# Kernel optimization log

Measured on AMD Instinct MI355X. Metric: run time of the kernel, lower is better.

The kernel has to match this reference:

```python
import jax, jax.numpy as jnp
import numpy as np

N_TILES, NX = 6, 96
IN_C, HID_C = 128, 256
BATCH = 4


def _build_neighbors(n_tiles=N_TILES, nx=NX):
    # 4-connectivity on each tile with periodic wrap (fixed cubed-sphere-style
    # grid graph; preserves the gather/mean access pattern of build_dgl_graph).
    i, j = np.meshgrid(np.arange(nx), np.arange(nx), indexing='ij')
    idx = lambda ii, jj: (ii % nx) * nx + (jj % nx)
    per_tile = np.stack([idx(i - 1, j), idx(i + 1, j), idx(i, j - 1), idx(i, j + 1)],
                        axis=-1).reshape(nx * nx, 4)
    offsets = (np.arange(n_tiles) * nx * nx)[:, None, None]
    return (per_tile[None] + offsets).reshape(-1, 4).astype(np.int32)


def setup_inputs() -> dict:
    key = jax.random.key(0)
    ks = jax.random.split(key, 6)
    s = lambda fan_in: 1.0 / np.sqrt(fan_in)
    return {
        'x': jax.random.normal(ks[0], (BATCH, N_TILES, NX, NX, IN_C), jnp.float32),
        'neighbors': jnp.asarray(_build_neighbors()),
        'W_self1': jax.random.normal(ks[1], (IN_C, HID_C), jnp.float32) * s(IN_C),
        'W_neigh1': jax.random.normal(ks[2], (IN_C, HID_C), jnp.float32) * s(IN_C),
        'b1': jnp.zeros((HID_C,), jnp.float32),
        'W_self2': jax.random.normal(ks[3], (HID_C, HID_C), jnp.float32) * s(HID_C),
        'W_neigh2': jax.random.normal(ks[4], (HID_C, HID_C), jnp.float32) * s(HID_C),
        'b2': jnp.zeros((HID_C,), jnp.float32),
    }


def _sage_conv(h, neighbors, W_self, W_neigh, b):
    # h: [B, N, C]; neighbors: [N, 4] -> mean-aggregated SAGEConv
    h_neigh = jnp.mean(h[:, neighbors], axis=2)  # [B, N, 4, C] -> [B, N, C]
    return jnp.einsum('bnc,cd->bnd', h, W_self) + \
           jnp.einsum('bnc,cd->bnd', h_neigh, W_neigh) + b


def reference(x, neighbors, W_self1, W_neigh1, b1, W_self2, W_neigh2, b2):
    B, T, X, Y, C = x.shape
    h = x.reshape(B, T * X * Y, C)                      # flatten sphere -> nodes
    h = jax.nn.relu(_sage_conv(h, neighbors, W_self1, W_neigh1, b1))
    h = jax.nn.relu(_sage_conv(h, neighbors, W_self2, W_neigh2, b2))
    return h.reshape(B, T, X, Y, -1)
```

## Files before the change

### kernel.cpp

```cpp
#include <hip/hip_runtime.h>
#include <stdint.h>

typedef __attribute__((ext_vector_type(8))) short short8;
typedef __attribute__((ext_vector_type(4))) float f32x4;

#define NNODES 55296
#define DOUT 256

#define WAIT_VM(N) asm volatile("s_waitcnt vmcnt(" #N ")" ::: "memory")
#define SOFT_FENCE asm volatile("" ::: "memory")

__device__ __forceinline__ float bf2f(unsigned short h) {
    union { unsigned u; float f; } x; x.u = ((unsigned)h) << 16; return x.f;
}
__device__ __forceinline__ unsigned short f2bf(float f) {
    union { float f; unsigned u; } x; x.f = f;
    return (unsigned short)((x.u + 0x7fffu + ((x.u >> 16) & 1u)) >> 16);
}

__device__ __forceinline__ void storev(float* p, float v) { *p = v; }
__device__ __forceinline__ void storev(unsigned short* p, float v) { *p = f2bf(v); }

__device__ __forceinline__ void dma16(const void* g, void* l) {
    __builtin_amdgcn_global_load_lds(
        reinterpret_cast<const unsigned int __attribute__((address_space(1)))*>((uintptr_t)g),
        reinterpret_cast<unsigned int __attribute__((address_space(3)))*>((uintptr_t)l),
        16, 0, 0);
}

__device__ __forceinline__ short8 frag_self(const float* p) {
    float4 a = *(const float4*)p, b = *(const float4*)(p + 4);
    union { short8 s; unsigned short u[8]; } r;
    r.u[0] = f2bf(a.x); r.u[1] = f2bf(a.y); r.u[2] = f2bf(a.z); r.u[3] = f2bf(a.w);
    r.u[4] = f2bf(b.x); r.u[5] = f2bf(b.y); r.u[6] = f2bf(b.z); r.u[7] = f2bf(b.w);
    return r.s;
}
__device__ __forceinline__ short8 frag_self(const unsigned short* p) {
    return *(const short8*)p;
}
__device__ __forceinline__ void acc8(const float* p, float* o) {
    float4 a = *(const float4*)p, b = *(const float4*)(p + 4);
    o[0] += a.x; o[1] += a.y; o[2] += a.z; o[3] += a.w;
    o[4] += b.x; o[5] += b.y; o[6] += b.z; o[7] += b.w;
}
__device__ __forceinline__ void acc8(const unsigned short* p, float* o) {
    uint4 v = *(const uint4*)p;
    const unsigned short* u = (const unsigned short*)&v;
#pragma unroll
    for (int i = 0; i < 8; ++i) o[i] += bf2f(u[i]);
}
template <typename TIN>
__device__ __forceinline__ short8 frag_mean4(const TIN* p0, const TIN* p1,
                                             const TIN* p2, const TIN* p3) {
    float s[8] = {0.f, 0.f, 0.f, 0.f, 0.f, 0.f, 0.f, 0.f};
    acc8(p0, s); acc8(p1, s); acc8(p2, s); acc8(p3, s);
    union { short8 s8; unsigned short u[8]; } r;
#pragma unroll
    for (int i = 0; i < 8; ++i) r.u[i] = f2bf(s[i] * 0.25f);
    return r.s8;
}

__global__ void build_wt(const float* __restrict__ Ws,
                         const float* __restrict__ Wn,
                         unsigned short* __restrict__ Wt, int C) {
    int K2 = 2 * C;
    int idx = blockIdx.x * 256 + threadIdx.x;
    if (idx >= 256 * K2) return;
    int d = idx / K2;
    int k = idx - d * K2;
    float v = (k < C) ? Ws[(size_t)k * DOUT + d] : Wn[(size_t)(k - C) * DOUT + d];
    Wt[idx] = f2bf(v);
}

__global__ __launch_bounds__(256) void mean_xb(const float* __restrict__ x,
                                               const int* __restrict__ nbr,
                                               unsigned short* __restrict__ xm) {
    const int idx = blockIdx.x * 256 + threadIdx.x;
    const int node = idx >> 4;
    const int ch = (idx & 15) * 8;
    const int b = node / NNODES;
    const int n = node - b * NNODES;
    const size_t bbase = (size_t)b * NNODES;
    const int4 nb = *(const int4*)(nbr + (size_t)n * 4);
    const float* ps = x + (size_t)node * 128 + ch;
    union { uint4 v; unsigned short u[8]; } rs, rm;
    float4 a0 = *(const float4*)ps, a1 = *(const float4*)(ps + 4);
    rs.u[0] = f2bf(a0.x); rs.u[1] = f2bf(a0.y); rs.u[2] = f2bf(a0.z); rs.u[3] = f2bf(a0.w);
    rs.u[4] = f2bf(a1.x); rs.u[5] = f2bf(a1.y); rs.u[6] = f2bf(a1.z); rs.u[7] = f2bf(a1.w);
    float s[8] = {0.f, 0.f, 0.f, 0.f, 0.f, 0.f, 0.f, 0.f};
    acc8(x + (bbase + nb.x) * 128 + ch, s);
    acc8(x + (bbase + nb.y) * 128 + ch, s);
    acc8(x + (bbase + nb.z) * 128 + ch, s);
    acc8(x + (bbase + nb.w) * 128 + ch, s);
#pragma unroll
    for (int i = 0; i < 8; ++i) rm.u[i] = f2bf(s[i] * 0.25f);
    *(uint4*)(xm + (size_t)node * 256 + ch) = rs.v;
    *(uint4*)(xm + (size_t)node * 256 + 128 + ch) = rm.v;
}

template <int C, typename TIN>
__global__ __launch_bounds__(256) void mean_pass(const TIN* __restrict__ hin,
                                                 const int* __restrict__ nbr,
                                                 unsigned short* __restrict__ hm) {
    constexpr int CPL = C / 8;
    const int idx = blockIdx.x * 256 + threadIdx.x;
    const int node = idx / CPL;
    const int ch = (idx - node * CPL) * 8;
    const int b = node / NNODES;
    const int n = node - b * NNODES;
    const size_t bbase = (size_t)b * NNODES;
    const int4 nb = *(const int4*)(nbr + (size_t)n * 4);
    float s[8] = {0.f, 0.f, 0.f, 0.f, 0.f, 0.f, 0.f, 0.f};
    acc8(hin + (bbase + nb.x) * (size_t)C + ch, s);
    acc8(hin + (bbase + nb.y) * (size_t)C + ch, s);
    acc8(hin + (bbase + nb.z) * (size_t)C + ch, s);
    acc8(hin + (bbase + nb.w) * (size_t)C + ch, s);
    union { uint4 v; unsigned short u[8]; } r;
#pragma unroll
    for (int i = 0; i < 8; ++i) r.u[i] = f2bf(s[i] * 0.25f);
    *(uint4*)(hm + (size_t)node * C + ch) = r.v;
}

template <int NK, typename TOUT>
__global__ __launch_bounds__(256) void sage_v13(
    const unsigned short* __restrict__ h1p,
    const unsigned short* __restrict__ hmp,
    const unsigned short* __restrict__ Wt,
    const float* __restrict__ bias,
    TOUT* __restrict__ out,
    int nwg) {
    extern __shared__ char lds[];
    constexpr int WB = NK * 64;
    const int tid = threadIdx.x;
    const int bid = blockIdx.x;
    const int wk = (bid & 7) * (nwg >> 3) + (bid >> 3);
    const int yg = wk & 1;
    const int rb = wk >> 1;
    const int gcol0 = yg * 128;
    const int rowbase = rb * 128;

    const int l = tid & 63, w = tid >> 6;
    const int lr = l & 15, lg = l >> 4;
    const int rowg = w >> 1;
    const int colb = (w & 1) * 64;

    const char* wsrc = (const char*)Wt + (size_t)gcol0 * WB;

    auto stageW = [&](int q) {
        char* wb = lds + ((q & 1) << 14);
#pragma unroll
        for (int i = 0; i < 4; ++i) {
            int o = w * 1024 + i * 4096 + l * 16;
            int col = o >> 7, kq = o & 127;
            dma16(wsrc + (unsigned)(col * WB + q * 128 + (kq ^ ((col & 7) << 4))),
                  wb + o);
        }
    };
    auto issueA = [&](int p) {
        const char* base = (NK == 16 && p >= 8) ? (const char*)hmp : (const char*)h1p;
        const unsigned kb = (unsigned)(p & 7) * 64;
        char* ring = lds + 32768 + (p & 3) * 8192;
#pragma unroll
        for (int i = 0; i < 2; ++i) {
            const int cj = w + i * 4;
            const int row = rowbase + cj * 16 + lr;
            dma16(base + ((unsigned)row * 512 + kb + (unsigned)(lg << 4)),
                  ring + cj * 1024);
        }
    };

    stageW(0); issueA(0); issueA(1); issueA(2);

    f32x4 acc[4][4];
#pragma unroll
    for (int m = 0; m < 4; ++m)
#pragma unroll
        for (int j = 0; j < 4; ++j) acc[m][j] = (f32x4){0.f, 0.f, 0.f, 0.f};

    const int abase = rowg * 4096 + lg * 256 + lr * 16;

#pragma unroll
    for (int kk = 0; kk < NK; ++kk) {
        int n;
        if (kk == 0) n = 4;
        else if (kk & 1) n = ((kk + 1 < NK) ? 6 : 0) + ((kk + 2 < NK) ? 2 : 0);
        else n = 2 + ((kk + 2 < NK) ? 2 : 0);
        switch (n) {
            case 0: WAIT_VM(0); break;
            case 2: WAIT_VM(2); break;
            case 4: WAIT_VM(4); break;
            case 6: WAIT_VM(6); break;
            default: WAIT_VM(8); break;
        }
        __builtin_amdgcn_s_barrier();
        SOFT_FENCE;

        if (((kk & 1) == 0) && (kk + 2 < NK)) stageW((kk + 2) >> 1);
        if (kk + 3 < NK) issueA(kk + 3);

        const int bufo = 32768 + (kk & 3) * 8192;
        short8 af[4];
#pragma unroll
        for (int m = 0; m < 4; ++m)
            af[m] = *(const short8*)(lds + bufo + abase + m * 1024);

        char* wbuf = lds + (((kk >> 1) & 1) << 14);
        const int kq0 = ((kk & 1) << 6) | (lg << 4);
#pragma unroll
        for (int j = 0; j < 4; ++j) {
            const int col = colb + j * 16 + lr;
            const short8 wf = *(const short8*)(
                wbuf + (col << 7) + (kq0 ^ ((lr & 7) << 4)));
#pragma unroll
            for (int m = 0; m < 4; ++m)
                acc[m][j] = __builtin_amdgcn_mfma_f32_16x16x32_bf16(wf, af[m], acc[m][j], 0, 0, 0);
        }
        SOFT_FENCE;
    }

#pragma unroll
    for (int m = 0; m < 4; ++m) {
        const int row = rowbase + rowg * 64 + m * 16 + lr;
#pragma unroll
        for (int j = 0; j < 4; ++j) {
            const int gcol = gcol0 + colb + j * 16 + lg * 4;
            const float4 bv = *(const float4*)(bias + gcol);
            float o0 = fmaxf(acc[m][j][0] + bv.x, 0.f);
            float o1 = fmaxf(acc[m][j][1] + bv.y, 0.f);
            float o2 = fmaxf(acc[m][j][2] + bv.z, 0.f);
            float o3 = fmaxf(acc[m][j][3] + bv.w, 0.f);
            if constexpr (sizeof(TOUT) == 4) {
                float4 o = {o0, o1, o2, o3};
                *(float4*)((float*)out + (size_t)row * 256 + gcol) = o;
            } else {
                union { unsigned short u[4]; uint2 v; } pk;
                pk.u[0] = f2bf(o0); pk.u[1] = f2bf(o1);
                pk.u[2] = f2bf(o2); pk.u[3] = f2bf(o3);
                *(uint2*)((unsigned short*)out + (size_t)row * 256 + gcol) = pk.v;
            }
        }
    }
}

template <int C, typename TIN, typename TOUT>
__global__ __launch_bounds__(512, 2) void sage_v3(
    const TIN* __restrict__ hin, const int* __restrict__ nbr,
    const unsigned short* __restrict__ Wt, const float* __restrict__ bias,
    TOUT* __restrict__ out) {
    constexpr int K2 = 2 * C;
    constexpr int ROWB = K2 * 2;
    constexpr int LCOLS = 131072 / ROWB;
    constexpr int CG = LCOLS / 128;
    constexpr int RG = 8 / CG;
    extern __shared__ char Bs[];

    const int tid = threadIdx.x;
    const int gcol0 = blockIdx.y * LCOLS;
    {
        const char* src = (const char*)(Wt + (size_t)gcol0 * K2);
#pragma unroll
        for (int i = 0; i < 16; ++i) {
            int byt = (i * 512 + tid) * 16;
            uint4 v = *(const uint4*)(src + byt);
            int c = byt / ROWB;
            *(uint4*)(Bs + (byt ^ ((c & 7) << 4))) = v;
        }
    }
    __syncthreads();

    const int l = tid & 63;
    const int w = tid >> 6;
    const int rowg = w / CG;
    const int colb = (w % CG) * 128;
    const int lr = l & 15, lg = l >> 4;

    const int rowbase = blockIdx.x * (RG * 64) + rowg * 64;
    const int bb = rowbase / NNODES;
    const int n0 = rowbase - bb * NNODES;
    const size_t bbase = (size_t)bb * NNODES;

    unsigned soff[4], noff[4][4];
#pragma unroll
    for (int m = 0; m < 4; ++m) {
        int r = m * 16 + lr;
        soff[m] = (unsigned)(((rowbase + r) * (size_t)C + lg * 8) * sizeof(TIN));
        int4 nb = *(const int4*)(nbr + (size_t)(n0 + r) * 4);
        noff[m][0] = (unsigned)(((bbase + nb.x) * C + lg * 8) * sizeof(TIN));
        noff[m][1] = (unsigned)(((bbase + nb.y) * C + lg * 8) * sizeof(TIN));
        noff[m][2] = (unsigned)(((bbase + nb.z) * C + lg * 8) * sizeof(TIN));
        noff[m][3] = (unsigned)(((bbase + nb.w) * C + lg * 8) * sizeof(TIN));
    }
    const char* hb = (const char*)hin;

    f32x4 acc[4][8];
#pragma unroll
    for (int m = 0; m < 4; ++m)
#pragma unroll
        for (int j = 0; j < 8; ++j) acc[m][j] = (f32x4){0.f, 0.f, 0.f, 0.f};

#pragma unroll
    for (int kk = 0; kk < K2 / 32; ++kk) {
        const int k0 = kk * 32;
        short8 a[4];
        if (k0 < C) {
            const unsigned kb = k0 * sizeof(TIN);
#pragma unroll
            for (int m = 0; m < 4; ++m)
                a[m] = frag_self((const TIN*)(hb + soff[m] + kb));
        } else {
            const unsigned kb = (k0 - C) * sizeof(TIN);
#pragma unroll
            for (int m = 0; m < 4; ++m)
                a[m] = frag_mean4((const TIN*)(hb + noff[m][0] + kb),
                                  (const TIN*)(hb + noff[m][1] + kb),
                                  (const TIN*)(hb + noff[m][2] + kb),
                                  (const TIN*)(hb + noff[m][3] + kb));
        }
#pragma unroll
        for (int j = 0; j < 8; ++j) {
            const int c = colb + j * 16 + lr;
            const short8 bf = *(const short8*)(
                Bs + ((c * ROWB + (k0 + lg * 8) * 2) ^ ((l & 7) << 4)));
#pragma unroll
            for (int m = 0; m < 4; ++m)
                acc[m][j] = __builtin_amdgcn_mfma_f32_16x16x32_bf16(a[m], bf, acc[m][j], 0, 0, 0);
        }
    }

#pragma unroll
    for (int j = 0; j < 8; ++j) {
        const int gcol = gcol0 + colb + j * 16 + lr;
        const float bv = bias[gcol];
#pragma unroll
        for (int m = 0; m < 4; ++m) {
#pragma unroll
            for (int r = 0; r < 4; ++r) {
                const int row = rowbase + m * 16 + lg * 4 + r;
                storev(out + (size_t)row * DOUT + gcol, fmaxf(acc[m][j][r] + bv, 0.f));
            }
        }
    }
}

extern "C" void kernel_launch(void* const* d_in, const int* in_sizes, int n_in,
                              void* d_out, int out_size, void* d_ws, size_t ws_size,
                              hipStream_t stream) {
    const float* x = (const float*)d_in[0];
    const int* nbr = (const int*)d_in[1];
    const float* Ws1 = (const float*)d_in[2];
    const float* Wn1 = (const float*)d_in[3];
    const float* b1 = (const float*)d_in[4];
    const float* Ws2 = (const float*)d_in[5];
    const float* Wn2 = (const float*)d_in[6];
    const float* b2 = (const float*)d_in[7];
    float* out = (float*)d_out;

    const int B = in_sizes[0] / (NNODES * 128);
    const int M = B * NNODES;

    char* ws = (char*)d_ws;
    const size_t h1_bytes = (size_t)M * DOUT * 2;
    const size_t hm_bytes = (size_t)M * DOUT * 2;
    const size_t need = h1_bytes + hm_bytes + 131072 + 262144;

    if (ws_size >= need) {
        unsigned short* h1 = (unsigned short*)ws;
        unsigned short* xm = (unsigned short*)(ws + h1_bytes);
        unsigned short* Wt1 = (unsigned short*)(ws + h1_bytes + hm_bytes);
        unsigned short* Wt2 = Wt1 + 256 * 256;

        build_wt<<<256, 256, 0, stream>>>(Ws1, Wn1, Wt1, 128);
        build_wt<<<512, 256, 0, stream>>>(Ws2, Wn2, Wt2, 256);

        hipFuncSetAttribute((const void*)sage_v13<8, unsigned short>,
                            hipFuncAttributeMaxDynamicSharedMemorySize, 65536);
        hipFuncSetAttribute((const void*)sage_v13<16, float>,
                            hipFuncAttributeMaxDynamicSharedMemorySize, 65536);

        const int nwg = (M / 128) * 2;

        mean_xb<<<M / 16, 256, 0, stream>>>(x, nbr, xm);
        sage_v13<8, unsigned short>
            <<<nwg, 256, 65536, stream>>>(xm, xm, Wt1, b1, h1, nwg);
        mean_pass<256, unsigned short><<<M * 32 / 256, 256, 0, stream>>>(h1, nbr, xm);
        sage_v13<16, float>
            <<<nwg, 256, 65536, stream>>>(h1, xm, Wt2, b2, out, nwg);
    } else {
        unsigned short* h1 = (unsigned short*)ws;
        unsigned short* Wt1 = (unsigned short*)(ws + h1_bytes);
        unsigned short* Wt2 = Wt1 + 256 * 256;

        build_wt<<<256, 256, 0, stream>>>(Ws1, Wn1, Wt1, 128);
        build_wt<<<512, 256, 0, stream>>>(Ws2, Wn2, Wt2, 256);

        hipFuncSetAttribute((const void*)sage_v3<128, float, unsigned short>,
                            hipFuncAttributeMaxDynamicSharedMemorySize, 131072);
        hipFuncSetAttribute((const void*)sage_v3<256, unsigned short, float>,
                            hipFuncAttributeMaxDynamicSharedMemorySize, 131072);

        sage_v3<128, float, unsigned short>
            <<<dim3(M / 256, 1), 512, 131072, stream>>>(x, nbr, Wt1, b1, h1);
        sage_v3<256, unsigned short, float>
            <<<dim3(M / 512, 2), 512, 131072, stream>>>(h1, nbr, Wt2, b2, out);
    }
}
```

Measured before the change: 346.1 us.

## Store activations and weights in panel-major layout for contiguous DMA tiles

```diff
diff --git a/kernel.cpp b/kernel.cpp
--- a/kernel.cpp
+++ b/kernel.cpp
@@ -72,9 +72,25 @@
     Wt[idx] = f2bf(v);
 }
 
-__global__ __launch_bounds__(256) void mean_xb(const float* __restrict__ x,
-                                               const int* __restrict__ nbr,
-                                               unsigned short* __restrict__ xm) {
+__global__ void build_wt_pm(const float* __restrict__ Ws,
+                            const float* __restrict__ Wn,
+                            unsigned short* __restrict__ Wp, int C) {
+    int K2 = 2 * C;
+    int idx = blockIdx.x * 256 + threadIdx.x;
+    if (idx >= 256 * K2) return;
+    int d = idx / K2;
+    int k = idx - d * K2;
+    float v = (k < C) ? Ws[(size_t)k * DOUT + d] : Wn[(size_t)(k - C) * DOUT + d];
+    int q = k >> 6;
+    int kqb = (k & 63) * 2;
+    int byte = q * 32768 + d * 128 + (kqb ^ ((d & 7) << 4));
+    Wp[byte >> 1] = f2bf(v);
+}
+
+__global__ __launch_bounds__(256) void mean_xb_pm(const float* __restrict__ x,
+                                                  const int* __restrict__ nbr,
+                                                  unsigned short* __restrict__ xm,
+                                                  int mTot) {
     const int idx = blockIdx.x * 256 + threadIdx.x;
     const int node = idx >> 4;
     const int ch = (idx & 15) * 8;
@@ -94,43 +110,44 @@
     acc8(x + (bbase + nb.w) * 128 + ch, s);
 #pragma unroll
     for (int i = 0; i < 8; ++i) rm.u[i] = f2bf(s[i] * 0.25f);
-    *(uint4*)(xm + (size_t)node * 256 + ch) = rs.v;
-    *(uint4*)(xm + (size_t)node * 256 + 128 + ch) = rm.v;
-}
-
-template <int C, typename TIN>
-__global__ __launch_bounds__(256) void mean_pass(const TIN* __restrict__ hin,
-                                                 const int* __restrict__ nbr,
-                                                 unsigned short* __restrict__ hm) {
-    constexpr int CPL = C / 8;
+    const size_t cs = (size_t)mTot * 32;
+    *(uint4*)(xm + (size_t)(ch >> 5) * cs + (size_t)node * 32 + (ch & 31)) = rs.v;
+    *(uint4*)(xm + (size_t)(4 + (ch >> 5)) * cs + (size_t)node * 32 + (ch & 31)) = rm.v;
+}
+
+__global__ __launch_bounds__(256) void mean_pass_pm(const unsigned short* __restrict__ h1,
+                                                    const int* __restrict__ nbr,
+                                                    unsigned short* __restrict__ hm,
+                                                    int mTot) {
     const int idx = blockIdx.x * 256 + threadIdx.x;
-    const int node = idx / CPL;
-    const int ch = (idx - node * CPL) * 8;
+    const int node = idx >> 5;
+    const int ch = (idx & 31) * 8;
     const int b = node / NNODES;
     const int n = node - b * NNODES;
     const size_t bbase = (size_t)b * NNODES;
     const int4 nb = *(const int4*)(nbr + (size_t)n * 4);
+    const size_t cs = (size_t)mTot * 32;
+    const size_t co = (size_t)(ch >> 5) * cs + (ch & 31);
     float s[8] = {0.f, 0.f, 0.f, 0.f, 0.f, 0.f, 0.f, 0.f};
-    acc8(hin + (bbase + nb.x) * (size_t)C + ch, s);
-    acc8(hin + (bbase + nb.y) * (size_t)C + ch, s);
-    acc8(hin + (bbase + nb.z) * (size_t)C + ch, s);
-    acc8(hin + (bbase + nb.w) * (size_t)C + ch, s);
+    acc8(h1 + co + (bbase + nb.x) * 32, s);
+    acc8(h1 + co + (bbase + nb.y) * 32, s);
+    acc8(h1 + co + (bbase + nb.z) * 32, s);
+    acc8(h1 + co + (bbase + nb.w) * 32, s);
     union { uint4 v; unsigned short u[8]; } r;
 #pragma unroll
     for (int i = 0; i < 8; ++i) r.u[i] = f2bf(s[i] * 0.25f);
-    *(uint4*)(hm + (size_t)node * C + ch) = r.v;
+    *(uint4*)(hm + co + (size_t)node * 32) = r.v;
 }
 
 template <int NK, typename TOUT>
-__global__ __launch_bounds__(256) void sage_v13(
-    const unsigned short* __restrict__ h1p,
-    const unsigned short* __restrict__ hmp,
-    const unsigned short* __restrict__ Wt,
+__global__ __launch_bounds__(256) void sage_v14(
+    const unsigned short* __restrict__ a0p,
+    const unsigned short* __restrict__ a1p,
+    const unsigned short* __restrict__ Wp,
     const float* __restrict__ bias,
     TOUT* __restrict__ out,
-    int nwg) {
+    int nwg, int mTot) {
     extern __shared__ char lds[];
-    constexpr int WB = NK * 64;
     const int tid = threadIdx.x;
     const int bid = blockIdx.x;
     const int wk = (bid & 7) * (nwg >> 3) + (bid >> 3);
@@ -144,28 +161,25 @@
     const int rowg = w >> 1;
     const int colb = (w & 1) * 64;
 
-    const char* wsrc = (const char*)Wt + (size_t)gcol0 * WB;
+    const size_t chstride = (size_t)mTot * 64;
 
     auto stageW = [&](int q) {
         char* wb = lds + ((q & 1) << 14);
+        const char* src = (const char*)Wp + (size_t)q * 32768 + (size_t)gcol0 * 128;
 #pragma unroll
         for (int i = 0; i < 4; ++i) {
-            int o = w * 1024 + i * 4096 + l * 16;
-            int col = o >> 7, kq = o & 127;
-            dma16(wsrc + (unsigned)(col * WB + q * 128 + (kq ^ ((col & 7) << 4))),
-                  wb + o);
+            int o = w * 4096 + i * 1024;
+            dma16(src + o + l * 16, wb + o + l * 16);
         }
     };
     auto issueA = [&](int p) {
-        const char* base = (NK == 16 && p >= 8) ? (const char*)hmp : (const char*)h1p;
-        const unsigned kb = (unsigned)(p & 7) * 64;
+        const char* base = (NK == 16 && p >= 8) ? (const char*)a1p : (const char*)a0p;
+        const char* src = base + (size_t)(p & 7) * chstride + (size_t)rowbase * 64;
         char* ring = lds + 32768 + (p & 3) * 8192;
 #pragma unroll
         for (int i = 0; i < 2; ++i) {
-            const int cj = w + i * 4;
-            const int row = rowbase + cj * 16 + lr;
-            dma16(base + ((unsigned)row * 512 + kb + (unsigned)(lg << 4)),
-                  ring + cj * 1024);
+            int o = w * 2048 + i * 1024;
+            dma16(src + o + l * 16, ring + o + l * 16);
         }
     };
 
@@ -176,8 +190,6 @@
     for (int m = 0; m < 4; ++m)
 #pragma unroll
         for (int j = 0; j < 4; ++j) acc[m][j] = (f32x4){0.f, 0.f, 0.f, 0.f};
-
-    const int abase = rowg * 4096 + lg * 256 + lr * 16;
 
 #pragma unroll
     for (int kk = 0; kk < NK; ++kk) {
@@ -202,7 +214,8 @@
         short8 af[4];
 #pragma unroll
         for (int m = 0; m < 4; ++m)
-            af[m] = *(const short8*)(lds + bufo + abase + m * 1024);
+            af[m] = *(const short8*)(lds + bufo +
+                                     ((rowg * 4 + m) * 16 + lr) * 64 + lg * 16);
 
         char* wbuf = lds + (((kk >> 1) & 1) << 14);
         const int kq0 = ((kk & 1) << 6) | (lg << 4);
@@ -236,7 +249,10 @@
                 union { unsigned short u[4]; uint2 v; } pk;
                 pk.u[0] = f2bf(o0); pk.u[1] = f2bf(o1);
                 pk.u[2] = f2bf(o2); pk.u[3] = f2bf(o3);
-                *(uint2*)((unsigned short*)out + (size_t)row * 256 + gcol) = pk.v;
+                unsigned short* hp = (unsigned short*)out +
+                    (size_t)(gcol >> 5) * ((size_t)mTot * 32) +
+                    (size_t)row * 32 + (gcol & 31);
+                *(uint2*)hp = pk.v;
             }
         }
     }
@@ -366,25 +382,25 @@
     if (ws_size >= need) {
         unsigned short* h1 = (unsigned short*)ws;
         unsigned short* xm = (unsigned short*)(ws + h1_bytes);
-        unsigned short* Wt1 = (unsigned short*)(ws + h1_bytes + hm_bytes);
-        unsigned short* Wt2 = Wt1 + 256 * 256;
-
-        build_wt<<<256, 256, 0, stream>>>(Ws1, Wn1, Wt1, 128);
-        build_wt<<<512, 256, 0, stream>>>(Ws2, Wn2, Wt2, 256);
-
-        hipFuncSetAttribute((const void*)sage_v13<8, unsigned short>,
+        unsigned short* W1p = (unsigned short*)(ws + h1_bytes + hm_bytes);
+        unsigned short* W2p = W1p + 256 * 256;
+
+        build_wt_pm<<<256, 256, 0, stream>>>(Ws1, Wn1, W1p, 128);
+        build_wt_pm<<<512, 256, 0, stream>>>(Ws2, Wn2, W2p, 256);
+
+        hipFuncSetAttribute((const void*)sage_v14<8, unsigned short>,
                             hipFuncAttributeMaxDynamicSharedMemorySize, 65536);
-        hipFuncSetAttribute((const void*)sage_v13<16, float>,
+        hipFuncSetAttribute((const void*)sage_v14<16, float>,
                             hipFuncAttributeMaxDynamicSharedMemorySize, 65536);
 
         const int nwg = (M / 128) * 2;
 
-        mean_xb<<<M / 16, 256, 0, stream>>>(x, nbr, xm);
-        sage_v13<8, unsigned short>
-            <<<nwg, 256, 65536, stream>>>(xm, xm, Wt1, b1, h1, nwg);
-        mean_pass<256, unsigned short><<<M * 32 / 256, 256, 0, stream>>>(h1, nbr, xm);
-        sage_v13<16, float>
-            <<<nwg, 256, 65536, stream>>>(h1, xm, Wt2, b2, out, nwg);
+        mean_xb_pm<<<M / 16, 256, 0, stream>>>(x, nbr, xm, M);
+        sage_v14<8, unsigned short>
+            <<<nwg, 256, 65536, stream>>>(xm, xm, W1p, b1, h1, nwg, M);
+        mean_pass_pm<<<M / 8, 256, 0, stream>>>(h1, nbr, xm, M);
+        sage_v14<16, float>
+            <<<nwg, 256, 65536, stream>>>(h1, xm, W2p, b2, out, nwg, M);
     } else {
         unsigned short* h1 = (unsigned short*)ws;
         unsigned short* Wt1 = (unsigned short*)(ws + h1_bytes);
```

After: 320.7 us. 7.3% less time.
